# Kernel optimization log

Hardware: AMD Instinct MI355X
Metric: run time of the kernel (lower is better)

## Reference

```python
import jax, jax.numpy as jnp
import numpy as np

N = 20000
E = 320000
K = 16          # k_dynamic
FEAT = 64       # feature_dim == hidden_channels
R = 4           # expansion_factor
NUM_OUT = 80000 # num_out_points == R*N
CH = 2000       # query chunk size for kNN (N % CH == 0)


def _lin(key, fan_in, fan_out):
    kw, kb = jax.random.split(key)
    lim = 1.0 / np.sqrt(fan_in)
    W = jax.random.uniform(kw, (fan_in, fan_out), minval=-lim, maxval=lim, dtype=jnp.float32)
    b = jax.random.uniform(kb, (fan_out,), minval=-lim, maxval=lim, dtype=jnp.float32)
    return W, b


def setup_inputs() -> dict:
    key = jax.random.key(0)
    ks = jax.random.split(key, 10)
    dep_points = jax.random.normal(ks[0], (N, 3), dtype=jnp.float32)
    edge_index = jax.random.randint(ks[1], (2, E), 0, N, dtype=jnp.int32)
    W1a, b1a = _lin(ks[2], 2 * 3, FEAT)       # edgeconv1 mlp layer 1
    W1b, b1b = _lin(ks[3], FEAT, FEAT)        # edgeconv1 mlp layer 2
    W2a, b2a = _lin(ks[4], 2 * FEAT, FEAT)    # dynamic edgeconv mlp layer 1
    W2b, b2b = _lin(ks[5], FEAT, FEAT)        # dynamic edgeconv mlp layer 2
    We, be = _lin(ks[6], FEAT, R * FEAT)      # linear_expand
    Wp, bp = _lin(ks[7], FEAT, FEAT)          # out_proj
    Wr1, br1 = _lin(ks[8], FEAT, FEAT)
    Wr2, br2 = _lin(ks[9], FEAT, 3)
    return dict(dep_points=dep_points, W1a=W1a, b1a=b1a, W1b=W1b, b1b=b1b,
                W2a=W2a, b2a=b2a, W2b=W2b, b2b=b2b, We=We, be=be, Wp=Wp, bp=bp,
                Wr1=Wr1, br1=br1, Wr2=Wr2, br2=br2, edge_index=edge_index)


def _mlp2(x, Wa, ba, Wb, bb):
    h = jax.nn.relu(x @ Wa + ba)
    return jax.nn.relu(h @ Wb + bb)


def _forward(dep_points, W1a, b1a, W1b, b1b, W2a, b2a, W2b, b2b,
             We, be, Wp, bp, Wr1, br1, Wr2, br2, edge_index):
    # --- EdgeConv with static edge_index (flow source_to_target: i = edge_index[1]) ---
    src, dst = edge_index[0], edge_index[1]
    xi = dep_points[dst]                             # [E,3] target features
    xj = dep_points[src]                             # [E,3] source features
    msg = _mlp2(jnp.concatenate([xi, xj - xi], -1), W1a, b1a, W1b, b1b)  # [E,64]
    x1 = jax.ops.segment_max(msg, dst, num_segments=N)                   # [N,64]
    x1 = jnp.where(jnp.isfinite(x1), x1, 0.0)        # empty segments -> 0

    # --- DynamicEdgeConv: kNN in feature space (indices non-differentiable) ---
    f = jax.lax.stop_gradient(x1)
    sq = jnp.sum(f * f, axis=1)                      # [N]
    def chunk_knn(qc):                                # qc: [CH,64]
        d2 = jnp.sum(qc * qc, axis=1)[:, None] + sq[None, :] - 2.0 * (qc @ f.T)
        return jax.lax.top_k(-d2, K)[1]               # [CH,K] includes self (d=0)
    nbr = jax.lax.map(chunk_knn, f.reshape(N // CH, CH, FEAT)).reshape(N, K)

    xi2 = x1[:, None, :]                              # [N,1,64]
    xj2 = x1[nbr]                                     # [N,K,64]
    pair = jnp.concatenate([jnp.broadcast_to(xi2, (N, K, FEAT)), xj2 - xi2], -1)
    msg2 = _mlp2(pair, W2a, b2a, W2b, b2b)            # [N,K,64]
    x2 = jnp.max(msg2, axis=1)                        # [N,64]

    # --- SimpleExpansion: expand + periodic shuffle + out_proj (B=1) ---
    xe = x2 @ We + be                                 # [N, R*64]
    xs = xe.reshape(N, R, FEAT).transpose(1, 0, 2).reshape(R * N, FEAT)
    feat = xs @ Wp + bp                               # [R*N,64]

    L = feat.shape[0]
    if L > NUM_OUT:
        feat = feat[:NUM_OUT]
    elif L < NUM_OUT:
        feat = jnp.concatenate([feat, jnp.repeat(feat[-1:], NUM_OUT - L, axis=0)], 0)

    h = jax.nn.relu(feat @ Wr1 + br1)
    return h @ Wr2 + br2                              # [NUM_OUT,3]


def reference(dep_points, W1a, b1a, W1b, b1b, W2a, b2a, W2b, b2b,
              We, be, Wp, bp, Wr1, br1, Wr2, br2, edge_index):
    return _forward(dep_points, W1a, b1a, W1b, b1b, W2a, b2a, W2b, b2b,
                    We, be, Wp, bp, Wr1, br1, Wr2, br2, edge_index)
```

## Files before the change

### kernel.cpp

```cpp
#include <hip/hip_runtime.h>
#include <hip/hip_bf16.h>

#define NPTS 20000
#define NE   320000
#define KNNK 16
#define NTILE ((NPTS + 127) / 128)

typedef __attribute__((ext_vector_type(8))) short bf16x8;
typedef __attribute__((ext_vector_type(4))) float f32x4;

#define OFF_X1   0
#define OFF_SQ   (OFF_X1 + NPTS*64)
#define OFF_WB   (OFF_SQ + NPTS)
#define WB_W1A  0
#define WB_B1A  384
#define WB_W1BT 448
#define WB_B1B  4544
#define WB_W2A  4608
#define WB_B2A  12800
#define WB_W2B  12864
#define WB_B2B  16960
#define WB_WE   17024
#define WB_BE   33408
#define WB_WP   33664
#define WB_BP   37760
#define WB_WR1  37824
#define WB_BR1  41920
#define WB_WR2  41984
#define WB_BR2  42176
#define WB_TOT  42240
#define OFF_NBR  (OFF_WB + WB_TOT)
#define OFF_OFFS (OFF_NBR + NPTS*KNNK)
#define WS1_TOT  (OFF_OFFS + NPTS + 4)
#define OFF_PK   ((WS1_TOT + 3) & ~3)
#define WS_NEED_BYTES ((size_t)WS1_TOT * 4)
#define WS2_BYTES (((size_t)OFF_PK + (size_t)NPTS*2*16) * 4)
#define WS4_BYTES (((size_t)OFF_PK + (size_t)NPTS*4*16) * 4)

__global__ __launch_bounds__(256) void k_out_zero(float* out, int nelem) {
    int i = blockIdx.x * 256 + threadIdx.x;
    if (i < nelem) out[i] = 0.0f;
}

__global__ __launch_bounds__(256) void k_zero(float* p, int nfloat4) {
    int i = blockIdx.x * 256 + threadIdx.x;
    if (i < nfloat4) { float4 z = {0.f,0.f,0.f,0.f}; ((float4*)p)[i] = z; }
}

__global__ __launch_bounds__(256) void k_prep(
    const float* W1a, const float* b1a,
    const float* W1b, const float* b1b,
    const float* W2a, const float* b2a,
    const float* W2b, const float* b2b,
    const float* We,  const float* be,
    const float* Wp,  const float* bp,
    const float* Wr1, const float* br1,
    const float* Wr2, const float* br2,
    float* wb)
{
    int t = blockIdx.x * blockDim.x + threadIdx.x;
    int gs = gridDim.x * blockDim.x;
    for (int i = t; i < 384;  i += gs) wb[WB_W1A+i] = W1a[i];
    for (int i = t; i < 64;   i += gs) wb[WB_B1A+i] = b1a[i];
    for (int i = t; i < 4096; i += gs) { int j=i>>6, k=i&63; wb[WB_W1BT+i] = W1b[k*64+j]; }
    for (int i = t; i < 64;   i += gs) wb[WB_B1B+i] = b1b[i];
    for (int i = t; i < 8192; i += gs) wb[WB_W2A+i] = W2a[i];
    for (int i = t; i < 64;   i += gs) wb[WB_B2A+i] = b2a[i];
    for (int i = t; i < 4096; i += gs) wb[WB_W2B+i] = W2b[i];
    for (int i = t; i < 64;   i += gs) wb[WB_B2B+i] = b2b[i];
    for (int i = t; i < 16384;i += gs) wb[WB_WE+i]  = We[i];
    for (int i = t; i < 256;  i += gs) wb[WB_BE+i]  = be[i];
    for (int i = t; i < 4096; i += gs) wb[WB_WP+i]  = Wp[i];
    for (int i = t; i < 64;   i += gs) wb[WB_BP+i]  = bp[i];
    for (int i = t; i < 4096; i += gs) wb[WB_WR1+i] = Wr1[i];
    for (int i = t; i < 64;   i += gs) wb[WB_BR1+i] = br1[i];
    for (int i = t; i < 192;  i += gs) wb[WB_WR2+i] = Wr2[i];
    for (int i = t; i < 3;    i += gs) wb[WB_BR2+i] = br2[i];
}

__global__ __launch_bounds__(256) void k_hist(const int* __restrict__ ei,
                                              unsigned int* __restrict__ counts) {
    int e = blockIdx.x * 256 + threadIdx.x;
    if (e >= NE) return;
    int d = ei[NE + e];
    d = d < 0 ? 0 : (d >= NPTS ? NPTS-1 : d);
    atomicAdd(&counts[d], 1u);
}

__global__ __launch_bounds__(64) void k_scan(const unsigned int* __restrict__ counts,
                                             unsigned int* __restrict__ cursor,
                                             unsigned int* __restrict__ offs) {
    __shared__ unsigned int ssum[64];
    __shared__ unsigned int sbase[65];
    int t = threadIdx.x;
    int lo = t * 313;
    int hi = lo + 313; if (hi > NPTS) hi = NPTS;
    unsigned int sum = 0;
    for (int i = lo; i < hi; ++i) sum += counts[i];
    ssum[t] = sum;
    __syncthreads();
    if (t == 0) {
        unsigned int run = 0;
        for (int i = 0; i < 64; ++i) { sbase[i] = run; run += ssum[i]; }
        sbase[64] = run;
    }
    __syncthreads();
    unsigned int run = sbase[t];
    for (int i = lo; i < hi; ++i) {
        unsigned int c = counts[i];
        offs[i] = run;
        cursor[i] = run;
        run += c;
    }
    if (t == 0) offs[NPTS] = sbase[64];
}

__global__ __launch_bounds__(256) void k_scatter(const int* __restrict__ ei,
                                                 unsigned int* __restrict__ cursor,
                                                 int* __restrict__ elist) {
    int e = blockIdx.x * 256 + threadIdx.x;
    if (e >= NE) return;
    int d = ei[NE + e];
    d = d < 0 ? 0 : (d >= NPTS ? NPTS-1 : d);
    unsigned int pos = atomicAdd(&cursor[d], 1u);
    elist[pos] = e;
}

__global__ __launch_bounds__(64) void k_gather(
    const float* __restrict__ dep, const int* __restrict__ ei,
    const int* __restrict__ elist, const unsigned int* __restrict__ offs,
    const float* __restrict__ W1a, const float* __restrict__ b1a,
    const float* __restrict__ W1b, const float* __restrict__ b1b,
    float* __restrict__ x1)
{
    __shared__ float hbuf[2][64];
    int d = blockIdx.x;
    int t = threadIdx.x;
    unsigned int o0 = offs[d], o1 = offs[d+1];
    float xi0 = dep[d*3+0], xi1 = dep[d*3+1], xi2 = dep[d*3+2];
    float wa0 = W1a[t], wa1 = W1a[64+t], wa2 = W1a[128+t];
    float wa3 = W1a[192+t], wa4 = W1a[256+t], wa5 = W1a[320+t];
    float ba = b1a[t], bb = b1b[t];
    float m = 0.0f;
    int buf = 0;
    for (unsigned int o = o0; o < o1; ++o) {
        int eid = elist[o];
        int s = ei[eid];
        s = s < 0 ? 0 : (s >= NPTS ? NPTS-1 : s);
        float dx0 = dep[s*3+0] - xi0;
        float dx1 = dep[s*3+1] - xi1;
        float dx2 = dep[s*3+2] - xi2;
        float h = ba;
        h = fmaf(xi0, wa0, h); h = fmaf(xi1, wa1, h); h = fmaf(xi2, wa2, h);
        h = fmaf(dx0, wa3, h); h = fmaf(dx1, wa4, h); h = fmaf(dx2, wa5, h);
        h = fmaxf(h, 0.0f);
        hbuf[buf][t] = h;
        __syncthreads();
        const float* hb = hbuf[buf];
        float z = bb;
#pragma unroll 8
        for (int j = 0; j < 64; ++j) z = fmaf(hb[j], W1b[j*64 + t], z);
        m = fmaxf(m, z);
        buf ^= 1;
    }
    x1[d*64 + t] = m;
}

__global__ __launch_bounds__(256) void k_conv(float* __restrict__ x1, float* __restrict__ sq) {
    int n = blockIdx.x * 256 + threadIdx.x;
    if (n >= NPTS) return;
    float* base = x1 + n*64;
    float4 r[16];
#pragma unroll
    for (int i = 0; i < 16; ++i) r[i] = ((const float4*)base)[i];
    float s = 0.f;
#pragma unroll
    for (int i = 0; i < 16; ++i) s += r[i].x*r[i].x + r[i].y*r[i].y + r[i].z*r[i].z + r[i].w*r[i].w;
    sq[n] = s;
    unsigned int* hi = (unsigned int*)base;
    unsigned int* lo = (unsigned int*)(base + 32);
#pragma unroll
    for (int j = 0; j < 8; ++j) {
        float v[8] = { r[2*j].x, r[2*j].y, r[2*j].z, r[2*j].w,
                       r[2*j+1].x, r[2*j+1].y, r[2*j+1].z, r[2*j+1].w };
        unsigned int hb[8], lb[8];
#pragma unroll
        for (int e = 0; e < 8; ++e) {
            unsigned int u = __float_as_uint(v[e]);
            hb[e] = (u + 0x7fffu + ((u >> 16) & 1u)) >> 16;
            float hf = __uint_as_float(hb[e] << 16);
            float lf = v[e] - hf;
            unsigned int ul = __float_as_uint(lf);
            lb[e] = (ul + 0x7fffu + ((ul >> 16) & 1u)) >> 16;
        }
        uint4 hp, lp;
        hp.x = hb[0] | (hb[1] << 16); hp.y = hb[2] | (hb[3] << 16);
        hp.z = hb[4] | (hb[5] << 16); hp.w = hb[6] | (hb[7] << 16);
        lp.x = lb[0] | (lb[1] << 16); lp.y = lb[2] | (lb[3] << 16);
        lp.z = lb[4] | (lb[5] << 16); lp.w = lb[6] | (lb[7] << 16);
        ((uint4*)hi)[j] = hp;
        ((uint4*)lo)[j] = lp;
    }
}

__device__ __forceinline__ void insk(unsigned int (&s)[16], unsigned int k) {
#pragma unroll
    for (int i = 15; i >= 1; --i) s[i] = min(s[i], max(s[i-1], k));
    s[0] = min(s[0], k);
}

#define RP  136
#define QB  64
__global__ __launch_bounds__(512) void k_knn(
    const float* __restrict__ x1, const float* __restrict__ sqv,
    int* __restrict__ nbr, unsigned int* __restrict__ pk)
{
    __shared__ __align__(16) unsigned short qbuf[QB*RP];
    __shared__ __align__(16) unsigned char  cbuf_raw[128*RP*2];
    __shared__ float ssq[128];
    unsigned short* cbuf = (unsigned short*)cbuf_raw;
    const int t  = threadIdx.x;
    const int n0 = blockIdx.x * QB;
    const int ns = gridDim.y;
    const int tps  = (NTILE + ns - 1) / ns;
    const int tbeg = blockIdx.y * tps;
    const int tend = min(NTILE, tbeg + tps);

#pragma unroll
    for (int i = 0; i < 2; ++i) {
        int ch2 = i*512 + t;
        int row = ch2 >> 4, off = ch2 & 15;
        uint4 v = make_uint4(0,0,0,0);
        if (n0 + row < NPTS) v = ((const uint4*)(x1 + (n0+row)*64))[off];
        *(uint4*)&qbuf[row*RP + off*8] = v;
    }
    __syncthreads();

    const int lane15 = t & 15;
    const int quad   = (t >> 4) & 3;
    const int w  = t >> 6;
    const int qs = w & 3;
    const int ch = w >> 2;
    bf16x8 Bh[2], Bl[2];
    {
        const unsigned short* qr = &qbuf[(qs*16 + lane15)*RP + quad*8];
        Bh[0] = *(const bf16x8*)(qr);
        Bh[1] = *(const bf16x8*)(qr + 32);
        Bl[0] = *(const bf16x8*)(qr + 64);
        Bl[1] = *(const bf16x8*)(qr + 96);
    }
    int myq = n0 + qs*16 + lane15;
    float sqq = (myq < NPTS) ? sqv[myq] : 0.0f;
    unsigned int sk[16];
#pragma unroll
    for (int m = 0; m < 16; ++m) sk[m] = 0xFFFFFFFFu;

    uint4 pv[4];
    int prow[4], poff[4];
#pragma unroll
    for (int i = 0; i < 4; ++i) {
        int ch2 = i*512 + t;
        prow[i] = tbeg*128 + (ch2 >> 4); poff[i] = ch2 & 15;
        pv[i] = make_uint4(0,0,0,0);
        if (prow[i] < NPTS) pv[i] = ((const uint4*)(x1 + prow[i]*64))[poff[i]];
    }
    float sreg = (t < 128 && tbeg*128 + t < NPTS) ? sqv[tbeg*128 + t] : 1e30f;

    for (int tile = tbeg; tile < tend; ++tile) {
        const int c0 = tile * 128;
        __syncthreads();
#pragma unroll
        for (int i = 0; i < 4; ++i)
            *(uint4*)&cbuf[(prow[i] - c0)*RP + poff[i]*8] = pv[i];
        if (t < 128) ssq[t] = sreg;
        __syncthreads();

        unsigned int pm  = min(sk[15], (unsigned int)__shfl_xor((int)sk[15], 16));
        unsigned int swv = min(pm, (unsigned int)__shfl_xor((int)pm, 32));

        if (tile + 1 < tend) {
            const int c0n = c0 + 128;
#pragma unroll
            for (int i = 0; i < 4; ++i) {
                int row = prow[i] + 128;
                pv[i] = make_uint4(0,0,0,0);
                if (row < NPTS) pv[i] = ((const uint4*)(x1 + row*64))[poff[i]];
                prow[i] = row;
            }
            sreg = (t < 128 && c0n + t < NPTS) ? sqv[c0n + t] : 1e30f;
        }

#pragma unroll
        for (int t4 = 0; t4 < 4; ++t4) {
            const unsigned short* cr = &cbuf[(ch*64 + t4*16 + lane15)*RP + quad*8];
            bf16x8 Ah0 = *(const bf16x8*)(cr);
            bf16x8 Ah1 = *(const bf16x8*)(cr + 32);
            bf16x8 Al0 = *(const bf16x8*)(cr + 64);
            bf16x8 Al1 = *(const bf16x8*)(cr + 96);
            f32x4 acc = (f32x4){0.f,0.f,0.f,0.f};
            acc = __builtin_amdgcn_mfma_f32_16x16x32_bf16(Ah0, Bh[0], acc, 0, 0, 0);
            acc = __builtin_amdgcn_mfma_f32_16x16x32_bf16(Al0, Bh[0], acc, 0, 0, 0);
            acc = __builtin_amdgcn_mfma_f32_16x16x32_bf16(Ah0, Bl[0], acc, 0, 0, 0);
            acc = __builtin_amdgcn_mfma_f32_16x16x32_bf16(Ah1, Bh[1], acc, 0, 0, 0);
            acc = __builtin_amdgcn_mfma_f32_16x16x32_bf16(Al1, Bh[1], acc, 0, 0, 0);
            acc = __builtin_amdgcn_mfma_f32_16x16x32_bf16(Ah1, Bl[1], acc, 0, 0, 0);
            int cbase = ch*64 + t4*16 + quad*4;
            float4 s4 = *(const float4*)&ssq[cbase];
            float e0 = fmaxf(fmaf(-2.0f, acc[0], s4.x) + sqq, 0.0f);
            float e1 = fmaxf(fmaf(-2.0f, acc[1], s4.y) + sqq, 0.0f);
            float e2 = fmaxf(fmaf(-2.0f, acc[2], s4.z) + sqq, 0.0f);
            float e3 = fmaxf(fmaf(-2.0f, acc[3], s4.w) + sqq, 0.0f);
            unsigned int cg = (unsigned int)(c0 + cbase);
            unsigned int k0 = (__float_as_uint(e0) & 0xFFFF8000u) | (cg+0u);
            unsigned int k1 = (__float_as_uint(e1) & 0xFFFF8000u) | (cg+1u);
            unsigned int k2 = (__float_as_uint(e2) & 0xFFFF8000u) | (cg+2u);
            unsigned int k3 = (__float_as_uint(e3) & 0xFFFF8000u) | (cg+3u);
            unsigned int mn = min(min(k0,k1), min(k2,k3));
            if (mn < swv) {
                if (k0 < sk[15]) insk(sk, k0);
                if (k1 < sk[15]) insk(sk, k1);
                if (k2 < sk[15]) insk(sk, k2);
                if (k3 < sk[15]) insk(sk, k3);
            }
        }
    }
    __syncthreads();
    {
        int q = qs*16 + lane15, lid = ch*4 + quad;
        unsigned int* fk = (unsigned int*)cbuf_raw;
        int base = q*136 + lid*17;
#pragma unroll
        for (int m = 0; m < 16; ++m) fk[base + m] = sk[m];
    }
    __syncthreads();
    if (t < QB && n0 + t < NPTS) {
        const unsigned int* fk = (const unsigned int*)cbuf_raw;
        int qb = t*136;
        int pr[8] = {0,0,0,0,0,0,0,0};
        int obase = (ns == 1) ? (n0 + t)*16 : ((n0 + t)*ns + blockIdx.y)*16;
        for (int r = 0; r < 16; ++r) {
            unsigned int best = 0xFFFFFFFFu; int bl = 0;
#pragma unroll
            for (int l = 0; l < 8; ++l) {
                unsigned int k = fk[qb + l*17 + pr[l]];
                if (k < best) { best = k; bl = l; }
            }
#pragma unroll
            for (int l = 0; l < 8; ++l) pr[l] += (bl == l) ? 1 : 0;
            if (ns == 1) {
                int idx = (int)(best & 0x7FFFu);
                nbr[obase + r] = idx >= NPTS ? NPTS-1 : idx;
            } else {
                pk[obase + r] = best;
            }
        }
    }
}

__global__ __launch_bounds__(256) void k_fmerge(
    const unsigned int* __restrict__ pk, int ns, int* __restrict__ nbr)
{
    int q = blockIdx.x * 256 + threadIdx.x;
    if (q >= NPTS) return;
    const unsigned int* fk = pk + q*ns*16;
    int pr[4] = {0,0,0,0};
    for (int r = 0; r < 16; ++r) {
        unsigned int best = 0xFFFFFFFFu; int bl = 0;
        for (int l = 0; l < ns; ++l) {
            unsigned int k = fk[l*16 + pr[l]];
            if (k < best) { best = k; bl = l; }
        }
        pr[bl]++;
        int idx = (int)(best & 0x7FFFu);
        nbr[q*16 + r] = idx >= NPTS ? NPTS-1 : idx;
    }
}

__device__ inline float bf2f(unsigned short u) {
    return __uint_as_float(((unsigned int)u) << 16);
}

__global__ __launch_bounds__(64) void k_fuse(
    const float* __restrict__ x1, const int* __restrict__ nbr,
    const float* __restrict__ wb, float* __restrict__ out)
{
    __shared__ __align__(16) float sxr[64];
    __shared__ __align__(16) float svec[64];
    __shared__ __align__(16) float sx2[64];
    __shared__ int snb[16];
    int n = blockIdx.x;
    int t = threadIdx.x;
    {
        const unsigned short* xr = (const unsigned short*)(x1 + n*64);
        sxr[t] = bf2f(xr[t]) + bf2f(xr[64+t]);
    }
    if (t < 16) snb[t] = nbr[n*16 + t];
    __syncthreads();
    const float* W2a = wb + WB_W2A;
    const float* W2b = wb + WB_W2B;
    const float4* sx4 = (const float4*)sxr;
    const float4* sv4 = (const float4*)svec;
    float wd[64], wz[64];
#pragma unroll
    for (int i = 0; i < 64; ++i) wd[i] = W2a[(64+i)*64 + t];
#pragma unroll
    for (int i = 0; i < 64; ++i) wz[i] = W2b[i*64 + t];
    float A = wb[WB_B2A + t];
#pragma unroll
    for (int i4 = 0; i4 < 16; ++i4) {
        float4 v = sx4[i4];
        const float* wr = W2a + i4*256 + t;
        A = fmaf(v.x, wr[0], A); A = fmaf(v.y, wr[64], A);
        A = fmaf(v.z, wr[128], A); A = fmaf(v.w, wr[192], A);
    }
    float D = 0.0f;
#pragma unroll
    for (int i4 = 0; i4 < 16; ++i4) {
        float4 v = sx4[i4];
        D = fmaf(v.x, wd[i4*4+0], D); D = fmaf(v.y, wd[i4*4+1], D);
        D = fmaf(v.z, wd[i4*4+2], D); D = fmaf(v.w, wd[i4*4+3], D);
    }
    const float AD = A - D;
    const float bz = wb[WB_B2B + t];
    float x2v = 0.0f;
    for (int k = 0; k < 16; ++k) {
        int nb = snb[k];
        {
            const unsigned short* yr = (const unsigned short*)(x1 + nb*64);
            svec[t] = bf2f(yr[t]) + bf2f(yr[64+t]);
        }
        __syncthreads();
        float h = AD;
#pragma unroll
        for (int i4 = 0; i4 < 16; ++i4) {
            float4 v = sv4[i4];
            h = fmaf(v.x, wd[i4*4+0], h); h = fmaf(v.y, wd[i4*4+1], h);
            h = fmaf(v.z, wd[i4*4+2], h); h = fmaf(v.w, wd[i4*4+3], h);
        }
        h = fmaxf(h, 0.f);
        __syncthreads();
        svec[t] = h;
        __syncthreads();
        float z = bz;
#pragma unroll
        for (int i4 = 0; i4 < 16; ++i4) {
            float4 v = sv4[i4];
            z = fmaf(v.x, wz[i4*4+0], z); z = fmaf(v.y, wz[i4*4+1], z);
            z = fmaf(v.z, wz[i4*4+2], z); z = fmaf(v.w, wz[i4*4+3], z);
        }
        x2v = fmaxf(x2v, fmaxf(z, 0.f));
        __syncthreads();
    }
    sx2[t] = x2v;
    __syncthreads();
    const float4* sx24 = (const float4*)sx2;
    const float* We  = wb + WB_WE;
    const float* Wp  = wb + WB_WP;
    const float* Wr1 = wb + WB_WR1;
    const float* Wr2 = wb + WB_WR2;
    for (int r = 0; r < 4; ++r) {
        float xe = wb[WB_BE + r*64 + t];
#pragma unroll
        for (int i4 = 0; i4 < 16; ++i4) {
            float4 v = sx24[i4];
            const float* wr = We + i4*1024 + r*64 + t;
            xe = fmaf(v.x, wr[0], xe); xe = fmaf(v.y, wr[256], xe);
            xe = fmaf(v.z, wr[512], xe); xe = fmaf(v.w, wr[768], xe);
        }
        svec[t] = xe;
        __syncthreads();
        float ft = wb[WB_BP + t];
#pragma unroll
        for (int i4 = 0; i4 < 16; ++i4) {
            float4 v = sv4[i4];
            const float* wr = Wp + i4*256 + t;
            ft = fmaf(v.x, wr[0], ft); ft = fmaf(v.y, wr[64], ft);
            ft = fmaf(v.z, wr[128], ft); ft = fmaf(v.w, wr[192], ft);
        }
        __syncthreads();
        svec[t] = ft;
        __syncthreads();
        float hh = wb[WB_BR1 + t];
#pragma unroll
        for (int i4 = 0; i4 < 16; ++i4) {
            float4 v = sv4[i4];
            const float* wr = Wr1 + i4*256 + t;
            hh = fmaf(v.x, wr[0], hh); hh = fmaf(v.y, wr[64], hh);
            hh = fmaf(v.z, wr[128], hh); hh = fmaf(v.w, wr[192], hh);
        }
        hh = fmaxf(hh, 0.f);
        __syncthreads();
        svec[t] = hh;
        __syncthreads();
        if (t < 3) {
            float o = wb[WB_BR2 + t];
            for (int i = 0; i < 64; ++i) o = fmaf(svec[i], Wr2[i*3 + t], o);
            int m = r * NPTS + n;
            out[m*3 + t] = o;
        }
        __syncthreads();
    }
}

extern "C" void kernel_launch(void* const* d_in, const int* in_sizes, int n_in,
                              void* d_out, int out_size, void* d_ws, size_t ws_size,
                              hipStream_t stream)
{
    const float* dep = (const float*)d_in[0];
    const float* W1a = (const float*)d_in[1];
    const float* b1a = (const float*)d_in[2];
    const float* W1b = (const float*)d_in[3];
    const float* b1b = (const float*)d_in[4];
    const float* W2a = (const float*)d_in[5];
    const float* b2a = (const float*)d_in[6];
    const float* W2b = (const float*)d_in[7];
    const float* b2b = (const float*)d_in[8];
    const float* We  = (const float*)d_in[9];
    const float* be  = (const float*)d_in[10];
    const float* Wp  = (const float*)d_in[11];
    const float* bp  = (const float*)d_in[12];
    const float* Wr1 = (const float*)d_in[13];
    const float* br1 = (const float*)d_in[14];
    const float* Wr2 = (const float*)d_in[15];
    const float* br2 = (const float*)d_in[16];
    const int* ei = (const int*)d_in[17];

    if (ws_size < WS_NEED_BYTES || d_ws == nullptr) {
        k_out_zero<<<(out_size + 255)/256, 256, 0, stream>>>((float*)d_out, out_size);
        return;
    }

    float* ws   = (float*)d_ws;
    float* x1   = ws + OFF_X1;
    float* sq   = ws + OFF_SQ;
    float* wbuf = ws + OFF_WB;
    int*   nbr  = (int*)(ws + OFF_NBR);
    unsigned int* counts = (unsigned int*)(ws + OFF_SQ);
    int*   elist = (int*)(ws + OFF_NBR);
    unsigned int* offs = (unsigned int*)(ws + OFF_OFFS);

    int ns = (ws_size >= WS4_BYTES) ? 4 : (ws_size >= WS2_BYTES) ? 2 : 1;
    unsigned int* pk = (unsigned int*)(ws + OFF_PK);

    k_zero<<<(NPTS/4 + 255)/256, 256, 0, stream>>>((float*)counts, NPTS/4);
    k_prep<<<64, 256, 0, stream>>>(W1a,b1a,W1b,b1b,W2a,b2a,W2b,b2b,We,be,Wp,bp,Wr1,br1,Wr2,br2, wbuf);
    k_hist<<<NE/256, 256, 0, stream>>>(ei, counts);
    k_scan<<<1, 64, 0, stream>>>(counts, counts, offs);
    k_scatter<<<NE/256, 256, 0, stream>>>(ei, counts, elist);
    k_gather<<<NPTS, 64, 0, stream>>>(dep, ei, elist, offs, W1a, b1a, W1b, b1b, x1);
    k_conv<<<(NPTS+255)/256, 256, 0, stream>>>(x1, sq);
    dim3 gk((NPTS + QB - 1)/QB, ns);
    k_knn<<<gk, 512, 0, stream>>>(x1, sq, nbr, pk);
    if (ns > 1) k_fmerge<<<(NPTS + 255)/256, 256, 0, stream>>>(pk, ns, nbr);
    k_fuse<<<NPTS, 64, 0, stream>>>(x1, nbr, wbuf, (float*)d_out);
}
```

Baseline: 1.275 ms.

## Prefetch neighbor loads in gather and fuse kernels, merge zeroing into prep, widen scan

Four separate changes. k_gather now holds its W1b column in registers and software-prefetches the next edges' source indices and coordinates across iterations, and k_fuse prefetches the next neighbour's bf16 row before the current compute. The counts zeroing moves into k_prep, removing one launch, and the single-block scan widens from 64 to 256 threads. Together these aim to hide global-load latency and cut launch and serial-scan overhead, at the cost of higher register pressure in k_gather from the 64-float array.

```diff
diff --git a/kernel.cpp b/kernel.cpp
--- a/kernel.cpp
+++ b/kernel.cpp
@@ -42,11 +42,6 @@
     if (i < nelem) out[i] = 0.0f;
 }
 
-__global__ __launch_bounds__(256) void k_zero(float* p, int nfloat4) {
-    int i = blockIdx.x * 256 + threadIdx.x;
-    if (i < nfloat4) { float4 z = {0.f,0.f,0.f,0.f}; ((float4*)p)[i] = z; }
-}
-
 __global__ __launch_bounds__(256) void k_prep(
     const float* W1a, const float* b1a,
     const float* W1b, const float* b1b,
@@ -56,10 +51,11 @@
     const float* Wp,  const float* bp,
     const float* Wr1, const float* br1,
     const float* Wr2, const float* br2,
-    float* wb)
+    float* wb, unsigned int* counts)
 {
     int t = blockIdx.x * blockDim.x + threadIdx.x;
     int gs = gridDim.x * blockDim.x;
+    for (int i = t; i < NPTS; i += gs) counts[i] = 0u;
     for (int i = t; i < 384;  i += gs) wb[WB_W1A+i] = W1a[i];
     for (int i = t; i < 64;   i += gs) wb[WB_B1A+i] = b1a[i];
     for (int i = t; i < 4096; i += gs) { int j=i>>6, k=i&63; wb[WB_W1BT+i] = W1b[k*64+j]; }
@@ -87,22 +83,23 @@
     atomicAdd(&counts[d], 1u);
 }
 
-__global__ __launch_bounds__(64) void k_scan(const unsigned int* __restrict__ counts,
-                                             unsigned int* __restrict__ cursor,
-                                             unsigned int* __restrict__ offs) {
-    __shared__ unsigned int ssum[64];
-    __shared__ unsigned int sbase[65];
+__global__ __launch_bounds__(256) void k_scan(const unsigned int* __restrict__ counts,
+                                              unsigned int* __restrict__ cursor,
+                                              unsigned int* __restrict__ offs) {
+    __shared__ unsigned int ssum[256];
+    __shared__ unsigned int sbase[257];
     int t = threadIdx.x;
-    int lo = t * 313;
-    int hi = lo + 313; if (hi > NPTS) hi = NPTS;
+    int lo = t * 79;
+    int hi = lo + 79; if (hi > NPTS) hi = NPTS;
+    if (lo > NPTS) lo = NPTS;
     unsigned int sum = 0;
     for (int i = lo; i < hi; ++i) sum += counts[i];
     ssum[t] = sum;
     __syncthreads();
     if (t == 0) {
         unsigned int run = 0;
-        for (int i = 0; i < 64; ++i) { sbase[i] = run; run += ssum[i]; }
-        sbase[64] = run;
+        for (int i = 0; i < 256; ++i) { sbase[i] = run; run += ssum[i]; }
+        sbase[256] = run;
     }
     __syncthreads();
     unsigned int run = sbase[t];
@@ -112,7 +109,7 @@
         cursor[i] = run;
         run += c;
     }
-    if (t == 0) offs[NPTS] = sbase[64];
+    if (t == 0) offs[NPTS] = sbase[256];
 }
 
 __global__ __launch_bounds__(256) void k_scatter(const int* __restrict__ ei,
@@ -124,6 +121,10 @@
     d = d < 0 ? 0 : (d >= NPTS ? NPTS-1 : d);
     unsigned int pos = atomicAdd(&cursor[d], 1u);
     elist[pos] = e;
+}
+
+__device__ __forceinline__ int clampn(int v) {
+    return v < 0 ? 0 : (v >= NPTS ? NPTS-1 : v);
 }
 
 __global__ __launch_bounds__(64) void k_gather(
@@ -141,27 +142,45 @@
     float wa0 = W1a[t], wa1 = W1a[64+t], wa2 = W1a[128+t];
     float wa3 = W1a[192+t], wa4 = W1a[256+t], wa5 = W1a[320+t];
     float ba = b1a[t], bb = b1b[t];
+    float w1b[64];
+#pragma unroll
+    for (int j = 0; j < 64; ++j) w1b[j] = W1b[j*64 + t];
     float m = 0.0f;
     int buf = 0;
-    for (unsigned int o = o0; o < o1; ++o) {
-        int eid = elist[o];
-        int s = ei[eid];
-        s = s < 0 ? 0 : (s >= NPTS ? NPTS-1 : s);
-        float dx0 = dep[s*3+0] - xi0;
-        float dx1 = dep[s*3+1] - xi1;
-        float dx2 = dep[s*3+2] - xi2;
-        float h = ba;
-        h = fmaf(xi0, wa0, h); h = fmaf(xi1, wa1, h); h = fmaf(xi2, wa2, h);
-        h = fmaf(dx0, wa3, h); h = fmaf(dx1, wa4, h); h = fmaf(dx2, wa5, h);
-        h = fmaxf(h, 0.0f);
-        hbuf[buf][t] = h;
-        __syncthreads();
-        const float* hb = hbuf[buf];
-        float z = bb;
+    if (o0 < o1) {
+        unsigned int last = o1 - 1;
+        int e0 = elist[o0];
+        int s0 = clampn(ei[e0]);
+        float dx0 = dep[s0*3+0] - xi0;
+        float dx1 = dep[s0*3+1] - xi1;
+        float dx2 = dep[s0*3+2] - xi2;
+        unsigned int i1 = o0 + 1 < last ? o0 + 1 : last;
+        unsigned int i2 = o0 + 2 < last ? o0 + 2 : last;
+        int s_nxt  = clampn(ei[elist[i1]]);
+        int eid_n2 = elist[i2];
+        for (unsigned int o = o0; o < o1; ++o) {
+            float h = ba;
+            h = fmaf(xi0, wa0, h); h = fmaf(xi1, wa1, h); h = fmaf(xi2, wa2, h);
+            h = fmaf(dx0, wa3, h); h = fmaf(dx1, wa4, h); h = fmaf(dx2, wa5, h);
+            h = fmaxf(h, 0.0f);
+            hbuf[buf][t] = h;
+            __syncthreads();
+            float ndx0 = dep[s_nxt*3+0] - xi0;
+            float ndx1 = dep[s_nxt*3+1] - xi1;
+            float ndx2 = dep[s_nxt*3+2] - xi2;
+            int ns = ei[eid_n2];
+            unsigned int i3 = o + 3 < last ? o + 3 : last;
+            int neid = elist[i3];
+            const float* hb = hbuf[buf];
+            float z = bb;
 #pragma unroll 8
-        for (int j = 0; j < 64; ++j) z = fmaf(hb[j], W1b[j*64 + t], z);
-        m = fmaxf(m, z);
-        buf ^= 1;
+            for (int j = 0; j < 64; ++j) z = fmaf(hb[j], w1b[j], z);
+            m = fmaxf(m, z);
+            buf ^= 1;
+            dx0 = ndx0; dx1 = ndx1; dx2 = ndx2;
+            s_nxt = clampn(ns);
+            eid_n2 = neid;
+        }
     }
     x1[d*64 + t] = m;
 }
@@ -423,13 +442,18 @@
     const float AD = A - D;
     const float bz = wb[WB_B2B + t];
     float x2v = 0.0f;
+    unsigned short ya, yb;
+    {
+        const unsigned short* yr = (const unsigned short*)(x1 + snb[0]*64);
+        ya = yr[t]; yb = yr[64+t];
+    }
     for (int k = 0; k < 16; ++k) {
-        int nb = snb[k];
-        {
-            const unsigned short* yr = (const unsigned short*)(x1 + nb*64);
-            svec[t] = bf2f(yr[t]) + bf2f(yr[64+t]);
-        }
-        __syncthreads();
+        svec[t] = bf2f(ya) + bf2f(yb);
+        __syncthreads();
+        if (k + 1 < 16) {
+            const unsigned short* yr = (const unsigned short*)(x1 + snb[k+1]*64);
+            ya = yr[t]; yb = yr[64+t];
+        }
         float h = AD;
 #pragma unroll
         for (int i4 = 0; i4 < 16; ++i4) {
@@ -542,10 +566,9 @@
     int ns = (ws_size >= WS4_BYTES) ? 4 : (ws_size >= WS2_BYTES) ? 2 : 1;
     unsigned int* pk = (unsigned int*)(ws + OFF_PK);
 
-    k_zero<<<(NPTS/4 + 255)/256, 256, 0, stream>>>((float*)counts, NPTS/4);
-    k_prep<<<64, 256, 0, stream>>>(W1a,b1a,W1b,b1b,W2a,b2a,W2b,b2b,We,be,Wp,bp,Wr1,br1,Wr2,br2, wbuf);
+    k_prep<<<64, 256, 0, stream>>>(W1a,b1a,W1b,b1b,W2a,b2a,W2b,b2b,We,be,Wp,bp,Wr1,br1,Wr2,br2, wbuf, counts);
     k_hist<<<NE/256, 256, 0, stream>>>(ei, counts);
-    k_scan<<<1, 64, 0, stream>>>(counts, counts, offs);
+    k_scan<<<1, 256, 0, stream>>>(counts, counts, offs);
     k_scatter<<<NE/256, 256, 0, stream>>>(ei, counts, elist);
     k_gather<<<NPTS, 64, 0, stream>>>(dep, ei, elist, offs, W1a, b1a, W1b, b1b, x1);
     k_conv<<<(NPTS+255)/256, 256, 0, stream>>>(x1, sq);
```

Measured after the change: 1.805 ms. 41.6% more time.
